# Kernel tuning notes

Hardware: AMD Instinct MI355X
Metric: run time of the kernel (lower is better)

The kernel has to match this reference:

```python
import jax, jax.numpy as jnp
import numpy as np

EPS = 1e-5

def _layernorm(x, gamma, beta):
    mu = jnp.mean(x, axis=-1, keepdims=True)
    var = jnp.var(x, axis=-1, keepdims=True)
    return (x - mu) * jax.lax.rsqrt(var + EPS) * gamma + beta

def setup_inputs() -> dict:
    key = jax.random.key(0)
    ks = jax.random.split(key, 8)
    B, I, H = 8192, 1024, 1024
    s_w = 1.0 / np.sqrt(I)
    s_u = 1.0 / np.sqrt(H)
    return {
        "x": jax.random.normal(ks[0], (B, I), jnp.float32),
        "h": jax.random.normal(ks[1], (B, H), jnp.float32),
        "c": jax.random.normal(ks[2], (B, H), jnp.float32),
        "W_w": jax.random.uniform(ks[3], (I, 4 * H), jnp.float32, -s_w, s_w),
        "W_b": jax.random.uniform(ks[4], (4 * H,), jnp.float32, -s_w, s_w),
        "U_w": jax.random.uniform(ks[5], (H, 4 * H), jnp.float32, -s_u, s_u),
        "ln_g_gamma": jnp.ones((4 * H,), jnp.float32),
        "ln_g_beta": jnp.zeros((4 * H,), jnp.float32),
        "ln_c_gamma": jnp.ones((H,), jnp.float32),
        "ln_c_beta": jnp.zeros((H,), jnp.float32),
    }

def reference(x, h, c, W_w, W_b, U_w, ln_g_gamma, ln_g_beta, ln_c_gamma, ln_c_beta):
    gates_x = x @ W_w + W_b            # [B, 4H]
    gates_h = h @ U_w                  # [B, 4H]
    gates = gates_x + gates_h + gates_x * gates_h  # multiplicative integration
    gates = _layernorm(gates, ln_g_gamma, ln_g_beta)
    i, f, g, o = jnp.split(gates, 4, axis=-1)
    i = jax.nn.sigmoid(i)
    f = jax.nn.sigmoid(f)
    o = jax.nn.sigmoid(o)
    g = jnp.tanh(g)
    c_new = f * c + i * g
    c_new = _layernorm(c_new, ln_c_gamma, ln_c_beta)
    h_new = o * jnp.tanh(c_new)
    return (h_new, h_new, c_new)
```

## Files before the change

kernel.cpp:

```cpp
#include <hip/hip_runtime.h>
#include <cstdint>


#define MB (1024ull * 1024ull)

typedef short bf16x8 __attribute__((ext_vector_type(8)));
typedef float f32x4  __attribute__((ext_vector_type(4)));

__device__ __forceinline__ bool bf16_mode(const void* g1) {
    return ((const unsigned short*)g1)[0] == 0x3F80u;
}
__device__ __forceinline__ float b2f(unsigned short u) {
    union { unsigned int i; float f; } v; v.i = ((unsigned int)u) << 16; return v.f;
}
__device__ __forceinline__ unsigned short f2b(float f) {
    unsigned int i = __float_as_uint(f);
    unsigned int r = (i + 0x7FFFu + ((i >> 16) & 1u)) >> 16;
    return (unsigned short)r;
}
__device__ __forceinline__ void up4(uint2 v, float* o) {
    o[0] = __uint_as_float(v.x << 16);
    o[1] = __uint_as_float(v.x & 0xFFFF0000u);
    o[2] = __uint_as_float(v.y << 16);
    o[3] = __uint_as_float(v.y & 0xFFFF0000u);
}
__device__ __forceinline__ unsigned int pack2(unsigned short a, unsigned short b) {
    return (unsigned int)a | ((unsigned int)b << 16);
}
__device__ __forceinline__ void ld4(const void* p, size_t idx, bool isbf, float* o) {
    if (isbf) up4(*(const uint2*)((const unsigned short*)p + idx), o);
    else { float4 v = *(const float4*)((const float*)p + idx); o[0]=v.x; o[1]=v.y; o[2]=v.z; o[3]=v.w; }
}
__device__ __forceinline__ float fast_sigmoid(float z) { return 1.f / (1.f + __expf(-z)); }
__device__ __forceinline__ float fast_tanh(float z)    { return 1.f - 2.f / (__expf(2.f * z) + 1.f); }

__device__ __forceinline__ void load_lds16(const unsigned short* g, unsigned short* l) {
    __builtin_amdgcn_global_load_lds(
        (const __attribute__((address_space(1))) unsigned int*)g,
        (__attribute__((address_space(3))) unsigned int*)l,
        16, 0, 0);
}

__global__ __launch_bounds__(256)
void prep_weights(const void* __restrict__ src, const void* __restrict__ g1,
                  unsigned short* __restrict__ dst)
{
    const bool isbf = bf16_mode(g1);
    __shared__ unsigned short tile[64][68];
    const int t  = threadIdx.x;
    const int tx = t & 15;
    const int ty = t >> 4;
    const int bx = blockIdx.x * 64;
    const int by = blockIdx.y * 64;
    if (isbf) {
        const unsigned short* s = (const unsigned short*)src;
#pragma unroll
        for (int it = 0; it < 4; ++it) {
            const int r = ty + it * 16;
            uint2 v = *(const uint2*)(s + (size_t)(by + r) * 4096 + bx + tx * 4);
            tile[r][tx * 4 + 0] = (unsigned short)(v.x & 0xFFFFu);
            tile[r][tx * 4 + 1] = (unsigned short)(v.x >> 16);
            tile[r][tx * 4 + 2] = (unsigned short)(v.y & 0xFFFFu);
            tile[r][tx * 4 + 3] = (unsigned short)(v.y >> 16);
        }
    } else {
        const float* s = (const float*)src;
#pragma unroll
        for (int it = 0; it < 4; ++it) {
            const int r = ty + it * 16;
            float4 v = *(const float4*)(s + (size_t)(by + r) * 4096 + bx + tx * 4);
            tile[r][tx * 4 + 0] = f2b(v.x);
            tile[r][tx * 4 + 1] = f2b(v.y);
            tile[r][tx * 4 + 2] = f2b(v.z);
            tile[r][tx * 4 + 3] = f2b(v.w);
        }
    }
    __syncthreads();
#pragma unroll
    for (int it = 0; it < 4; ++it) {
        const int rn = ty + it * 16;
        const int ck = tx * 4;
        uint2 w;
        w.x = pack2(tile[ck + 0][rn], tile[ck + 1][rn]);
        w.y = pack2(tile[ck + 2][rn], tile[ck + 3][rn]);
        *(uint2*)(dst + (size_t)(bx + rn) * 1024 + by + ck) = w;
    }
}

__global__ __launch_bounds__(256)
void prep_xh(const void* __restrict__ X, const void* __restrict__ Hs,
             const void* __restrict__ g1, void* __restrict__ outb)
{
    if (bf16_mode(g1)) return;
    const float* src = (blockIdx.y == 0) ? (const float*)X : (const float*)Hs;
    unsigned short* dst = (unsigned short*)((char*)outb + (blockIdx.y == 0 ? 48 * MB : 80 * MB));
    const size_t i0 = ((size_t)blockIdx.x * 256 + threadIdx.x) * 8;
    float4 a = *(const float4*)(src + i0);
    float4 b = *(const float4*)(src + i0 + 4);
    uint4 o;
    o.x = pack2(f2b(a.x), f2b(a.y));
    o.y = pack2(f2b(a.z), f2b(a.w));
    o.z = pack2(f2b(b.x), f2b(b.y));
    o.w = pack2(f2b(b.z), f2b(b.w));
    *(uint4*)(dst + i0) = o;
}

#define TM 128
#define TN 128
#define TK 32

__global__ __launch_bounds__(256, 2)
void milstm_gemm(const void* __restrict__ Xraw, const void* __restrict__ Hraw,
                 const void* __restrict__ g1, const void* __restrict__ Wbraw,
                 const void* __restrict__ outb,
                 const unsigned short* __restrict__ Wt,
                 const unsigned short* __restrict__ Ut,
                 unsigned short* __restrict__ G, int m0)
{
    const bool isbf = bf16_mode(g1);
    const unsigned short* X  = isbf ? (const unsigned short*)Xraw
                                    : (const unsigned short*)((const char*)outb + 48 * MB);
    const unsigned short* Hs = isbf ? (const unsigned short*)Hraw
                                    : (const unsigned short*)((const char*)outb + 80 * MB);

    __shared__ __align__(16) unsigned short sAx[TM * TK];
    __shared__ __align__(16) unsigned short sAh[TM * TK];
    __shared__ __align__(16) unsigned short sBw[TN * TK];
    __shared__ __align__(16) unsigned short sBu[TN * TK];

    const int tid  = threadIdx.x;
    const int wave = tid >> 6;
    const int lane = tid & 63;
    const int quad = lane >> 4;
    const int l16  = lane & 15;

    const int bm = blockIdx.y * TM;
    const int bn = blockIdx.x * TN;

    const int wm = (wave & 1) * 64;
    const int wn = (wave >> 1) * 64;

    const int c0   = wave * 2;
    const int srow = lane >> 2;
    const int skb  = (lane & 3) ^ ((srow >> 1) & 3);
    const int scol = skb * 8;

    const unsigned short* px0 = X  + (size_t)(m0 + bm + (c0 + 0) * 16 + srow) * 1024 + scol;
    const unsigned short* px1 = X  + (size_t)(m0 + bm + (c0 + 1) * 16 + srow) * 1024 + scol;
    const unsigned short* ph0 = Hs + (size_t)(m0 + bm + (c0 + 0) * 16 + srow) * 1024 + scol;
    const unsigned short* ph1 = Hs + (size_t)(m0 + bm + (c0 + 1) * 16 + srow) * 1024 + scol;
    const unsigned short* pw0 = Wt + (size_t)(bn + (c0 + 0) * 16 + srow) * 1024 + scol;
    const unsigned short* pw1 = Wt + (size_t)(bn + (c0 + 1) * 16 + srow) * 1024 + scol;
    const unsigned short* pu0 = Ut + (size_t)(bn + (c0 + 0) * 16 + srow) * 1024 + scol;
    const unsigned short* pu1 = Ut + (size_t)(bn + (c0 + 1) * 16 + srow) * 1024 + scol;

    unsigned short* dax0 = sAx + (c0 + 0) * 512;
    unsigned short* dax1 = sAx + (c0 + 1) * 512;
    unsigned short* dah0 = sAh + (c0 + 0) * 512;
    unsigned short* dah1 = sAh + (c0 + 1) * 512;
    unsigned short* dbw0 = sBw + (c0 + 0) * 512;
    unsigned short* dbw1 = sBw + (c0 + 1) * 512;
    unsigned short* dbu0 = sBu + (c0 + 0) * 512;
    unsigned short* dbu1 = sBu + (c0 + 1) * 512;

    const int kread = (quad ^ ((l16 >> 1) & 3)) * 8;

    f32x4 accx[4][4] = {};
    f32x4 acch[4][4] = {};

    for (int k0 = 0; k0 < 1024; k0 += TK) {
        load_lds16(px0 + k0, dax0);
        load_lds16(px1 + k0, dax1);
        load_lds16(ph0 + k0, dah0);
        load_lds16(ph1 + k0, dah1);
        load_lds16(pw0 + k0, dbw0);
        load_lds16(pw1 + k0, dbw1);
        load_lds16(pu0 + k0, dbu0);
        load_lds16(pu1 + k0, dbu1);
        __syncthreads();

        bf16x8 ax[4], ah[4];
#pragma unroll
        for (int mi = 0; mi < 4; ++mi) {
            ax[mi] = *(const bf16x8*)(sAx + (wm + mi * 16 + l16) * TK + kread);
            ah[mi] = *(const bf16x8*)(sAh + (wm + mi * 16 + l16) * TK + kread);
        }
#pragma unroll
        for (int ni = 0; ni < 4; ++ni) {
            bf16x8 bw = *(const bf16x8*)(sBw + (wn + ni * 16 + l16) * TK + kread);
            bf16x8 bu = *(const bf16x8*)(sBu + (wn + ni * 16 + l16) * TK + kread);
#pragma unroll
            for (int mi = 0; mi < 4; ++mi) {
                accx[mi][ni] = __builtin_amdgcn_mfma_f32_16x16x32_bf16(ax[mi], bw, accx[mi][ni], 0, 0, 0);
                acch[mi][ni] = __builtin_amdgcn_mfma_f32_16x16x32_bf16(ah[mi], bu, acch[mi][ni], 0, 0, 0);
            }
        }
        __syncthreads();
    }

#pragma unroll
    for (int ni = 0; ni < 4; ++ni) {
        const int col = bn + wn + ni * 16 + l16;
        const float bias = isbf ? b2f(((const unsigned short*)Wbraw)[col])
                                : ((const float*)Wbraw)[col];
#pragma unroll
        for (int mi = 0; mi < 4; ++mi) {
            const int row0 = bm + wm + mi * 16 + quad * 4;
#pragma unroll
            for (int r = 0; r < 4; ++r) {
                float gx = accx[mi][ni][r] + bias;
                float gh = acch[mi][ni][r];
                float gv = gx + gh + gx * gh;
                G[(size_t)(row0 + r) * 4096 + col] = f2b(gv);
            }
        }
    }
}

__global__ __launch_bounds__(256)
void milstm_cell(const unsigned short* __restrict__ G,
                 const void* __restrict__ C,
                 const void* __restrict__ g1, const void* __restrict__ b1,
                 const void* __restrict__ g2, const void* __restrict__ b2,
                 void* __restrict__ outb, int m0)
{
    const bool isbf = bf16_mode(g1);
    const int lrow = blockIdx.x;
    const int row  = m0 + lrow;
    const int tid  = threadIdx.x;
    const int lane = tid & 63;
    const int wave = tid >> 6;
    const unsigned short* grow = G + (size_t)lrow * 4096;

    __shared__ __align__(16) unsigned short srow[4096];
    __shared__ float red[16];

    float s = 0.f, ss = 0.f;
    const uint4* gv4 = (const uint4*)grow;
#pragma unroll
    for (int u = 0; u < 2; ++u) {
        uint4 v = gv4[tid * 2 + u];
        *(uint4*)(srow + (size_t)(tid * 2 + u) * 8) = v;
        unsigned int w[4] = { v.x, v.y, v.z, v.w };
#pragma unroll
        for (int q = 0; q < 4; ++q) {
            float flo = __uint_as_float(w[q] << 16);
            float fhi = __uint_as_float(w[q] & 0xFFFF0000u);
            s  += flo + fhi;
            ss += flo * flo + fhi * fhi;
        }
    }
#pragma unroll
    for (int off = 32; off > 0; off >>= 1) {
        s  += __shfl_xor(s, off, 64);
        ss += __shfl_xor(ss, off, 64);
    }
    if (lane == 0) { red[wave] = s; red[8 + wave] = ss; }
    __syncthreads();
    s  = red[0] + red[1] + red[2] + red[3];
    ss = red[8] + red[9] + red[10] + red[11];
    const float mu   = s * (1.f / 4096.f);
    const float rstd = rsqrtf(fmaxf(ss * (1.f / 4096.f) - mu * mu, 0.f) + 1e-5f);

    const int j0 = tid * 4;
    float xi[4], xf[4], xg[4], xo[4], cc[4];
    float G1[4], B1[4], ii[4], cn[4], ov[4];

    up4(*(const uint2*)(srow + j0),        xi);
    up4(*(const uint2*)(srow + 1024 + j0), xf);
    up4(*(const uint2*)(srow + 2048 + j0), xg);
    up4(*(const uint2*)(srow + 3072 + j0), xo);
    ld4(C, (size_t)row * 1024 + j0, isbf, cc);

    ld4(g1, j0, isbf, G1); ld4(b1, j0, isbf, B1);
#pragma unroll
    for (int q = 0; q < 4; ++q) ii[q] = fast_sigmoid((xi[q] - mu) * rstd * G1[q] + B1[q]);
    ld4(g1, 1024 + j0, isbf, G1); ld4(b1, 1024 + j0, isbf, B1);
#pragma unroll
    for (int q = 0; q < 4; ++q) xf[q] = fast_sigmoid((xf[q] - mu) * rstd * G1[q] + B1[q]);
    ld4(g1, 2048 + j0, isbf, G1); ld4(b1, 2048 + j0, isbf, B1);
#pragma unroll
    for (int q = 0; q < 4; ++q) xg[q] = fast_tanh((xg[q] - mu) * rstd * G1[q] + B1[q]);
    ld4(g1, 3072 + j0, isbf, G1); ld4(b1, 3072 + j0, isbf, B1);
#pragma unroll
    for (int q = 0; q < 4; ++q) ov[q] = fast_sigmoid((xo[q] - mu) * rstd * G1[q] + B1[q]);
#pragma unroll
    for (int q = 0; q < 4; ++q) cn[q] = xf[q] * cc[q] + ii[q] * xg[q];

    float s2  = cn[0] + cn[1] + cn[2] + cn[3];
    float ss2 = cn[0]*cn[0] + cn[1]*cn[1] + cn[2]*cn[2] + cn[3]*cn[3];
#pragma unroll
    for (int off = 32; off > 0; off >>= 1) {
        s2  += __shfl_xor(s2, off, 64);
        ss2 += __shfl_xor(ss2, off, 64);
    }
    if (lane == 0) { red[4 + wave] = s2; red[12 + wave] = ss2; }
    __syncthreads();
    s2  = red[4]  + red[5]  + red[6]  + red[7];
    ss2 = red[12] + red[13] + red[14] + red[15];
    const float mu2   = s2 * (1.f / 1024.f);
    const float rstd2 = rsqrtf(fmaxf(ss2 * (1.f / 1024.f) - mu2 * mu2, 0.f) + 1e-5f);

    ld4(g2, j0, isbf, G1);
    ld4(b2, j0, isbf, B1);

    float hv[4], cv[4];
#pragma unroll
    for (int q = 0; q < 4; ++q) {
        cv[q] = (cn[q] - mu2) * rstd2 * G1[q] + B1[q];
        hv[q] = ov[q] * fast_tanh(cv[q]);
    }

    const size_t BH = (size_t)8192 * 1024;
    if (isbf) {
        unsigned short* out = (unsigned short*)outb;
        uint2 hb, cb;
        hb.x = pack2(f2b(hv[0]), f2b(hv[1])); hb.y = pack2(f2b(hv[2]), f2b(hv[3]));
        cb.x = pack2(f2b(cv[0]), f2b(cv[1])); cb.y = pack2(f2b(cv[2]), f2b(cv[3]));
        *(uint2*)(out + (size_t)row * 1024 + j0)          = hb;
        *(uint2*)(out + BH + (size_t)row * 1024 + j0)     = hb;
        *(uint2*)(out + 2 * BH + (size_t)row * 1024 + j0) = cb;
    } else {
        float* out = (float*)outb;
        float4 hf = { hv[0], hv[1], hv[2], hv[3] };
        float4 cf = { cv[0], cv[1], cv[2], cv[3] };
        *(float4*)(out + (size_t)row * 1024 + j0)          = hf;
        *(float4*)(out + BH + (size_t)row * 1024 + j0)     = hf;
        *(float4*)(out + 2 * BH + (size_t)row * 1024 + j0) = cf;
    }
}

extern "C" void kernel_launch(void* const* d_in, const int* in_sizes, int n_in,
                              void* d_out, int out_size, void* d_ws, size_t ws_size,
                              hipStream_t stream)
{
    const void* X  = d_in[0];
    const void* Hh = d_in[1];
    const void* C  = d_in[2];
    const void* Ww = d_in[3];
    const void* Wb = d_in[4];
    const void* Uw = d_in[5];
    const void* g1 = d_in[6];
    const void* b1 = d_in[7];
    const void* g2 = d_in[8];
    const void* b2 = d_in[9];

    const bool single = ws_size >= 80 * MB;
    const size_t goff = single ? 64 * MB : 32 * MB;
    unsigned short* G  = (unsigned short*)d_ws;
    unsigned short* Wt = (unsigned short*)((char*)d_ws + goff);
    unsigned short* Ut = (unsigned short*)((char*)d_ws + goff + 8 * MB);

    prep_weights<<<dim3(64, 16), 256, 0, stream>>>(Ww, g1, Wt);
    prep_weights<<<dim3(64, 16), 256, 0, stream>>>(Uw, g1, Ut);
    prep_xh<<<dim3(4096, 2), 256, 0, stream>>>(X, Hh, g1, d_out);

    if (single) {
        milstm_gemm<<<dim3(32, 64), 256, 0, stream>>>(X, Hh, g1, Wb, d_out, Wt, Ut, G, 0);
        milstm_cell<<<dim3(8192), 256, 0, stream>>>(G, C, g1, b1, g2, b2, d_out, 0);
    } else {
        for (int ph = 0; ph < 2; ++ph) {
            const int m0 = ph * 4096;
            milstm_gemm<<<dim3(32, 32), 256, 0, stream>>>(X, Hh, g1, Wb, d_out, Wt, Ut, G, m0);
            milstm_cell<<<dim3(4096), 256, 0, stream>>>(G, C, g1, b1, g2, b2, d_out, m0);
        }
    }
}
```

Measured before the change: 407.0 us.

## Split x/h GEMMs into separate 256x256 pipelined tiles, move MI combine to cell kernel

Result: no change. 408.6 us (+0.4%).

```diff
diff --git a/kernel.cpp b/kernel.cpp
--- a/kernel.cpp
+++ b/kernel.cpp
@@ -1,4 +1,5 @@
 #include <hip/hip_runtime.h>
+#include <hip/hip_fp16.h>
 #include <cstdint>
 
 
@@ -17,6 +18,19 @@
     unsigned int i = __float_as_uint(f);
     unsigned int r = (i + 0x7FFFu + ((i >> 16) & 1u)) >> 16;
     return (unsigned short)r;
+}
+__device__ __forceinline__ unsigned short f2h(float f) {
+    __half h = __float2half_rn(f);
+    return *(unsigned short*)&h;
+}
+__device__ __forceinline__ void uph8(uint4 v, float* o) {
+    unsigned int w[4] = { v.x, v.y, v.z, v.w };
+#pragma unroll
+    for (int q = 0; q < 4; ++q) {
+        __half2 h = *(__half2*)&w[q];
+        float2 f = __half22float2(h);
+        o[2 * q] = f.x; o[2 * q + 1] = f.y;
+    }
 }
 __device__ __forceinline__ void up4(uint2 v, float* o) {
     o[0] = __uint_as_float(v.x << 16);
@@ -42,10 +56,13 @@
 }
 
 __global__ __launch_bounds__(256)
-void prep_weights(const void* __restrict__ src, const void* __restrict__ g1,
-                  unsigned short* __restrict__ dst)
+void prep_weights(const void* __restrict__ Ww, const void* __restrict__ Uw,
+                  const void* __restrict__ g1,
+                  unsigned short* __restrict__ Wt, unsigned short* __restrict__ Ut)
 {
     const bool isbf = bf16_mode(g1);
+    const void* src = blockIdx.z ? Uw : Ww;
+    unsigned short* dst = blockIdx.z ? Ut : Wt;
     __shared__ unsigned short tile[64][68];
     const int t  = threadIdx.x;
     const int tx = t & 15;
@@ -105,120 +122,103 @@
     *(uint4*)(dst + i0) = o;
 }
 
-#define TM 128
-#define TN 128
-#define TK 32
-
-__global__ __launch_bounds__(256, 2)
+__global__ __launch_bounds__(512, 2)
 void milstm_gemm(const void* __restrict__ Xraw, const void* __restrict__ Hraw,
-                 const void* __restrict__ g1, const void* __restrict__ Wbraw,
-                 const void* __restrict__ outb,
+                 const void* __restrict__ g1, const void* __restrict__ outb,
                  const unsigned short* __restrict__ Wt,
                  const unsigned short* __restrict__ Ut,
-                 unsigned short* __restrict__ G, int m0)
+                 unsigned short* __restrict__ Gx, unsigned short* __restrict__ Gh,
+                 int m0)
 {
     const bool isbf = bf16_mode(g1);
-    const unsigned short* X  = isbf ? (const unsigned short*)Xraw
-                                    : (const unsigned short*)((const char*)outb + 48 * MB);
-    const unsigned short* Hs = isbf ? (const unsigned short*)Hraw
-                                    : (const unsigned short*)((const char*)outb + 80 * MB);
-
-    __shared__ __align__(16) unsigned short sAx[TM * TK];
-    __shared__ __align__(16) unsigned short sAh[TM * TK];
-    __shared__ __align__(16) unsigned short sBw[TN * TK];
-    __shared__ __align__(16) unsigned short sBu[TN * TK];
-
-    const int tid  = threadIdx.x;
-    const int wave = tid >> 6;
-    const int lane = tid & 63;
+    const int  z    = blockIdx.z;
+    const unsigned short* A = z
+        ? (isbf ? (const unsigned short*)Hraw : (const unsigned short*)((const char*)outb + 80 * MB))
+        : (isbf ? (const unsigned short*)Xraw : (const unsigned short*)((const char*)outb + 48 * MB));
+    const unsigned short* Bm = z ? Ut : Wt;
+    unsigned short* Gout = z ? Gh : Gx;
+
+    __shared__ __align__(16) unsigned short lds[4][2][8192];
+
+    const int t    = threadIdx.x;
+    const int wave = t >> 6;
+    const int lane = t & 63;
     const int quad = lane >> 4;
     const int l16  = lane & 15;
-
-    const int bm = blockIdx.y * TM;
-    const int bn = blockIdx.x * TN;
-
-    const int wm = (wave & 1) * 64;
-    const int wn = (wave >> 1) * 64;
-
-    const int c0   = wave * 2;
-    const int srow = lane >> 2;
-    const int skb  = (lane & 3) ^ ((srow >> 1) & 3);
-    const int scol = skb * 8;
-
-    const unsigned short* px0 = X  + (size_t)(m0 + bm + (c0 + 0) * 16 + srow) * 1024 + scol;
-    const unsigned short* px1 = X  + (size_t)(m0 + bm + (c0 + 1) * 16 + srow) * 1024 + scol;
-    const unsigned short* ph0 = Hs + (size_t)(m0 + bm + (c0 + 0) * 16 + srow) * 1024 + scol;
-    const unsigned short* ph1 = Hs + (size_t)(m0 + bm + (c0 + 1) * 16 + srow) * 1024 + scol;
-    const unsigned short* pw0 = Wt + (size_t)(bn + (c0 + 0) * 16 + srow) * 1024 + scol;
-    const unsigned short* pw1 = Wt + (size_t)(bn + (c0 + 1) * 16 + srow) * 1024 + scol;
-    const unsigned short* pu0 = Ut + (size_t)(bn + (c0 + 0) * 16 + srow) * 1024 + scol;
-    const unsigned short* pu1 = Ut + (size_t)(bn + (c0 + 1) * 16 + srow) * 1024 + scol;
-
-    unsigned short* dax0 = sAx + (c0 + 0) * 512;
-    unsigned short* dax1 = sAx + (c0 + 1) * 512;
-    unsigned short* dah0 = sAh + (c0 + 0) * 512;
-    unsigned short* dah1 = sAh + (c0 + 1) * 512;
-    unsigned short* dbw0 = sBw + (c0 + 0) * 512;
-    unsigned short* dbw1 = sBw + (c0 + 1) * 512;
-    unsigned short* dbu0 = sBu + (c0 + 0) * 512;
-    unsigned short* dbu1 = sBu + (c0 + 1) * 512;
+    const int wm2  = wave >> 2;
+    const int wn4  = wave & 3;
+
+    const int nwg  = gridDim.x * gridDim.y;
+    const int wgid = blockIdx.y * gridDim.x + blockIdx.x;
+    const int swz  = (wgid & 7) * (nwg >> 3) + (wgid >> 3);
+    const int bm   = (swz >> 4) * 256;
+    const int bn   = (swz & 15) * 256;
+
+    const int kbsw = (((t & 3) ^ ((t >> 3) & 3)) * 8);
+    const unsigned short* sa0 = A  + (size_t)(m0 + bm + (t >> 2)) * 1024 + kbsw;
+    const unsigned short* sb0 = Bm + (size_t)(bn + (t >> 2)) * 1024 + kbsw;
+
+#define STAGE(tile, buf) do {                                        \
+        const int ko_ = (tile) * 32;                                 \
+        load_lds16(sa0 + ko_,          &lds[buf][0][t * 8]);         \
+        load_lds16(sa0 + 131072 + ko_, &lds[buf][0][4096 + t * 8]);  \
+        load_lds16(sb0 + ko_,          &lds[buf][1][t * 8]);         \
+        load_lds16(sb0 + 131072 + ko_, &lds[buf][1][4096 + t * 8]);  \
+    } while (0)
 
     const int kread = (quad ^ ((l16 >> 1) & 3)) * 8;
-
-    f32x4 accx[4][4] = {};
-    f32x4 acch[4][4] = {};
-
-    for (int k0 = 0; k0 < 1024; k0 += TK) {
-        load_lds16(px0 + k0, dax0);
-        load_lds16(px1 + k0, dax1);
-        load_lds16(ph0 + k0, dah0);
-        load_lds16(ph1 + k0, dah1);
-        load_lds16(pw0 + k0, dbw0);
-        load_lds16(pw1 + k0, dbw1);
-        load_lds16(pu0 + k0, dbu0);
-        load_lds16(pu1 + k0, dbu1);
-        __syncthreads();
-
-        bf16x8 ax[4], ah[4];
-#pragma unroll
-        for (int mi = 0; mi < 4; ++mi) {
-            ax[mi] = *(const bf16x8*)(sAx + (wm + mi * 16 + l16) * TK + kread);
-            ah[mi] = *(const bf16x8*)(sAh + (wm + mi * 16 + l16) * TK + kread);
+    const int raoff = (wm2 * 128 + l16) * 32 + kread;
+    const int rboff = (wn4 * 64 + l16) * 32 + kread;
+
+    f32x4 acc[8][4] = {};
+
+    STAGE(0, 0);
+    STAGE(1, 1);
+    STAGE(2, 2);
+
+    for (int q = 0; q < 32; ++q) {
+        const int buf = q & 3;
+        asm volatile("s_waitcnt vmcnt(8)" ::: "memory");
+        __builtin_amdgcn_s_barrier();
+        __builtin_amdgcn_sched_barrier(0);
+        STAGE((q + 3) & 31, (q + 3) & 3);
+
+        const unsigned short* pA = &lds[buf][0][0];
+        const unsigned short* pB = &lds[buf][1][0];
+        bf16x8 b[4], a[8];
+#pragma unroll
+        for (int ni = 0; ni < 4; ++ni) b[ni] = *(const bf16x8*)(pB + rboff + ni * 512);
+#pragma unroll
+        for (int mi = 0; mi < 8; ++mi) a[mi] = *(const bf16x8*)(pA + raoff + mi * 512);
+
+        __builtin_amdgcn_s_setprio(1);
+#pragma unroll
+        for (int mi = 0; mi < 8; ++mi)
+#pragma unroll
+            for (int ni = 0; ni < 4; ++ni)
+                acc[mi][ni] = __builtin_amdgcn_mfma_f32_16x16x32_bf16(a[mi], b[ni], acc[mi][ni], 0, 0, 0);
+        __builtin_amdgcn_s_setprio(0);
+    }
+#undef STAGE
+
+    const int col0 = bn + wn4 * 64 + l16;
+#pragma unroll
+    for (int mi = 0; mi < 8; ++mi) {
+        const int row0 = bm + wm2 * 128 + mi * 16 + quad * 4;
+#pragma unroll
+        for (int ni = 0; ni < 4; ++ni) {
+            const int col = col0 + ni * 16;
+#pragma unroll
+            for (int r = 0; r < 4; ++r)
+                Gout[(size_t)(row0 + r) * 4096 + col] = f2h(acc[mi][ni][r]);
         }
-#pragma unroll
-        for (int ni = 0; ni < 4; ++ni) {
-            bf16x8 bw = *(const bf16x8*)(sBw + (wn + ni * 16 + l16) * TK + kread);
-            bf16x8 bu = *(const bf16x8*)(sBu + (wn + ni * 16 + l16) * TK + kread);
-#pragma unroll
-            for (int mi = 0; mi < 4; ++mi) {
-                accx[mi][ni] = __builtin_amdgcn_mfma_f32_16x16x32_bf16(ax[mi], bw, accx[mi][ni], 0, 0, 0);
-                acch[mi][ni] = __builtin_amdgcn_mfma_f32_16x16x32_bf16(ah[mi], bu, acch[mi][ni], 0, 0, 0);
-            }
-        }
-        __syncthreads();
-    }
-
-#pragma unroll
-    for (int ni = 0; ni < 4; ++ni) {
-        const int col = bn + wn + ni * 16 + l16;
-        const float bias = isbf ? b2f(((const unsigned short*)Wbraw)[col])
-                                : ((const float*)Wbraw)[col];
-#pragma unroll
-        for (int mi = 0; mi < 4; ++mi) {
-            const int row0 = bm + wm + mi * 16 + quad * 4;
-#pragma unroll
-            for (int r = 0; r < 4; ++r) {
-                float gx = accx[mi][ni][r] + bias;
-                float gh = acch[mi][ni][r];
-                float gv = gx + gh + gx * gh;
-                G[(size_t)(row0 + r) * 4096 + col] = f2b(gv);
-            }
-        }
     }
 }
 
 __global__ __launch_bounds__(256)
-void milstm_cell(const unsigned short* __restrict__ G,
+void milstm_cell(const unsigned short* __restrict__ Gx,
+                 const unsigned short* __restrict__ Gh,
+                 const void* __restrict__ Wbr,
                  const void* __restrict__ C,
                  const void* __restrict__ g1, const void* __restrict__ b1,
                  const void* __restrict__ g2, const void* __restrict__ b2,
@@ -230,25 +230,32 @@
     const int tid  = threadIdx.x;
     const int lane = tid & 63;
     const int wave = tid >> 6;
-    const unsigned short* grow = G + (size_t)lrow * 4096;
-
-    __shared__ __align__(16) unsigned short srow[4096];
+    const uint4* gx4 = (const uint4*)(Gx + (size_t)lrow * 4096);
+    const uint4* gh4 = (const uint4*)(Gh + (size_t)lrow * 4096);
+
+    __shared__ __align__(16) float srow[4096];
     __shared__ float red[16];
 
     float s = 0.f, ss = 0.f;
-    const uint4* gv4 = (const uint4*)grow;
 #pragma unroll
     for (int u = 0; u < 2; ++u) {
-        uint4 v = gv4[tid * 2 + u];
-        *(uint4*)(srow + (size_t)(tid * 2 + u) * 8) = v;
-        unsigned int w[4] = { v.x, v.y, v.z, v.w };
-#pragma unroll
-        for (int q = 0; q < 4; ++q) {
-            float flo = __uint_as_float(w[q] << 16);
-            float fhi = __uint_as_float(w[q] & 0xFFFF0000u);
-            s  += flo + fhi;
-            ss += flo * flo + fhi * fhi;
+        const int gbase = (tid * 2 + u) * 8;
+        float fx[8], fh[8], bb[8];
+        uph8(gx4[tid * 2 + u], fx);
+        uph8(gh4[tid * 2 + u], fh);
+        ld4(Wbr, gbase, isbf, bb);
+        ld4(Wbr, gbase + 4, isbf, bb + 4);
+        float g[8];
+#pragma unroll
+        for (int k = 0; k < 8; ++k) {
+            const float ax = fx[k] + bb[k];
+            const float v  = ax + fh[k] + ax * fh[k];
+            g[k] = v;
+            s  += v;
+            ss += v * v;
         }
+        *(float4*)&srow[gbase]     = make_float4(g[0], g[1], g[2], g[3]);
+        *(float4*)&srow[gbase + 4] = make_float4(g[4], g[5], g[6], g[7]);
     }
 #pragma unroll
     for (int off = 32; off > 0; off >>= 1) {
@@ -263,13 +270,13 @@
     const float rstd = rsqrtf(fmaxf(ss * (1.f / 4096.f) - mu * mu, 0.f) + 1e-5f);
 
     const int j0 = tid * 4;
-    float xi[4], xf[4], xg[4], xo[4], cc[4];
+    float xi[4], xf[4], xg[4], cc[4];
     float G1[4], B1[4], ii[4], cn[4], ov[4];
 
-    up4(*(const uint2*)(srow + j0),        xi);
-    up4(*(const uint2*)(srow + 1024 + j0), xf);
-    up4(*(const uint2*)(srow + 2048 + j0), xg);
-    up4(*(const uint2*)(srow + 3072 + j0), xo);
+    { float4 v = *(const float4*)&srow[j0];        xi[0]=v.x; xi[1]=v.y; xi[2]=v.z; xi[3]=v.w; }
+    { float4 v = *(const float4*)&srow[1024 + j0]; xf[0]=v.x; xf[1]=v.y; xf[2]=v.z; xf[3]=v.w; }
+    { float4 v = *(const float4*)&srow[2048 + j0]; xg[0]=v.x; xg[1]=v.y; xg[2]=v.z; xg[3]=v.w; }
+    { float4 v = *(const float4*)&srow[3072 + j0]; ov[0]=v.x; ov[1]=v.y; ov[2]=v.z; ov[3]=v.w; }
     ld4(C, (size_t)row * 1024 + j0, isbf, cc);
 
     ld4(g1, j0, isbf, G1); ld4(b1, j0, isbf, B1);
@@ -283,7 +290,7 @@
     for (int q = 0; q < 4; ++q) xg[q] = fast_tanh((xg[q] - mu) * rstd * G1[q] + B1[q]);
     ld4(g1, 3072 + j0, isbf, G1); ld4(b1, 3072 + j0, isbf, B1);
 #pragma unroll
-    for (int q = 0; q < 4; ++q) ov[q] = fast_sigmoid((xo[q] - mu) * rstd * G1[q] + B1[q]);
+    for (int q = 0; q < 4; ++q) ov[q] = fast_sigmoid((ov[q] - mu) * rstd * G1[q] + B1[q]);
 #pragma unroll
     for (int q = 0; q < 4; ++q) cn[q] = xf[q] * cc[q] + ii[q] * xg[q];
 
@@ -345,24 +352,22 @@
     const void* g2 = d_in[8];
     const void* b2 = d_in[9];
 
-    const bool single = ws_size >= 80 * MB;
-    const size_t goff = single ? 64 * MB : 32 * MB;
-    unsigned short* G  = (unsigned short*)d_ws;
-    unsigned short* Wt = (unsigned short*)((char*)d_ws + goff);
-    unsigned short* Ut = (unsigned short*)((char*)d_ws + goff + 8 * MB);
-
-    prep_weights<<<dim3(64, 16), 256, 0, stream>>>(Ww, g1, Wt);
-    prep_weights<<<dim3(64, 16), 256, 0, stream>>>(Uw, g1, Ut);
+    const int P  = (ws_size >= 144 * MB) ? 1 : ((ws_size >= 80 * MB) ? 2 : 4);
+    const int MR = 8192 / P;
+    const size_t gsz = (size_t)MR * 4096;
+    unsigned short* Gx = (unsigned short*)d_ws;
+    unsigned short* Gh = Gx + gsz;
+    unsigned short* Wt = Gh + gsz;
+    unsigned short* Ut = Wt + (size_t)4096 * 1024;
+
+    prep_weights<<<dim3(64, 16, 2), 256, 0, stream>>>(Ww, Uw, g1, Wt, Ut);
     prep_xh<<<dim3(4096, 2), 256, 0, stream>>>(X, Hh, g1, d_out);
 
-    if (single) {
-        milstm_gemm<<<dim3(32, 64), 256, 0, stream>>>(X, Hh, g1, Wb, d_out, Wt, Ut, G, 0);
-        milstm_cell<<<dim3(8192), 256, 0, stream>>>(G, C, g1, b1, g2, b2, d_out, 0);
-    } else {
-        for (int ph = 0; ph < 2; ++ph) {
-            const int m0 = ph * 4096;
-            milstm_gemm<<<dim3(32, 32), 256, 0, stream>>>(X, Hh, g1, Wb, d_out, Wt, Ut, G, m0);
-            milstm_cell<<<dim3(4096), 256, 0, stream>>>(G, C, g1, b1, g2, b2, d_out, m0);
-        }
-    }
-}
+    for (int ph = 0; ph < P; ++ph) {
+        const int m0 = ph * MR;
+        milstm_gemm<<<dim3(16, MR / 256, 2), 512, 0, stream>>>(
+            X, Hh, g1, d_out, Wt, Ut, Gx, Gh, m0);
+        milstm_cell<<<dim3(MR), 256, 0, stream>>>(
+            Gx, Gh, Wb, C, g1, b1, g2, b2, d_out, m0);
+    }
+}
```
